# Kernel optimization log

Measured on AMD Instinct MI355X. Metric: run time of the kernel, lower is better.

The kernel has to match this reference:

```python
import jax, jax.numpy as jnp
import numpy as np

B, IN, HID, LAT, EH = 32768, 512, 2048, 128, 512
MID = max(HID // 2, LAT * 2)      # 1024
HALF = max(EH // 2, 4)            # 256
EPS = 1e-5
LN10 = float(np.log(10.0))


def setup_inputs() -> dict:
    key = jax.random.key(0)
    ks = jax.random.split(key, 24)
    r = lambda k, shp, s=0.02: (jax.random.normal(k, shp, dtype=jnp.float32) * s)
    d = {
        "x": jax.random.normal(ks[0], (B, IN), dtype=jnp.float32),
        "group_idx": jax.random.randint(ks[1], (B,), 0, 3),
        # encoder: Linear(IN,HID)+BN+ELU, Linear(HID,MID)+BN+ELU, Linear(MID,LAT)
        "e_w1": r(ks[2], (HID, IN)), "e_b1": jnp.zeros((HID,), jnp.float32),
        "e_g1": jnp.ones((HID,), jnp.float32), "e_be1": jnp.zeros((HID,), jnp.float32),
        "e_w2": r(ks[3], (MID, HID)), "e_b2": jnp.zeros((MID,), jnp.float32),
        "e_g2": jnp.ones((MID,), jnp.float32), "e_be2": jnp.zeros((MID,), jnp.float32),
        "e_w3": r(ks[4], (LAT, MID)), "e_b3": jnp.zeros((LAT,), jnp.float32),
        # shared: Linear(LAT+IN,HID)+BN+ELU, Linear(HID,MID)+BN+ELU
        "s_w1": r(ks[5], (HID, LAT + IN)), "s_b1": jnp.zeros((HID,), jnp.float32),
        "s_g1": jnp.ones((HID,), jnp.float32), "s_be1": jnp.zeros((HID,), jnp.float32),
        "s_w2": r(ks[6], (MID, HID)), "s_b2": jnp.zeros((MID,), jnp.float32),
        "s_g2": jnp.ones((MID,), jnp.float32), "s_be2": jnp.zeros((MID,), jnp.float32),
        # 3 expert heads, stacked on leading axis E=3
        "h_w1": r(ks[7], (3, EH, MID)), "h_b1": jnp.zeros((3, EH), jnp.float32),
        "h_w2": r(ks[8], (3, HALF, EH)), "h_b2": jnp.zeros((3, HALF), jnp.float32),
        "h_w3": r(ks[9], (3, HALF)), "h_b3": jnp.zeros((3,), jnp.float32),
    }
    return d


def _bn(h, g, b):
    # BatchNorm1d in training mode: batch mean, biased batch var
    m = jnp.mean(h, axis=0)
    v = jnp.var(h, axis=0)
    return (h - m) * (g / jnp.sqrt(v + EPS)) + b


def _elu(h):
    return jax.nn.elu(h)


def reference(x, group_idx,
              e_w1, e_b1, e_g1, e_be1, e_w2, e_b2, e_g2, e_be2, e_w3, e_b3,
              s_w1, s_b1, s_g1, s_be1, s_w2, s_b2, s_g2, s_be2,
              h_w1, h_b1, h_w2, h_b2, h_w3, h_b3):
    # encoder
    h = _elu(_bn(x @ e_w1.T + e_b1, e_g1, e_be1))
    h = _elu(_bn(h @ e_w2.T + e_b2, e_g2, e_be2))
    latent = h @ e_w3.T + e_b3                              # [B, LAT]
    # shared trunk
    z = jnp.concatenate([latent, x], axis=-1)               # [B, LAT+IN]
    h = _elu(_bn(z @ s_w1.T + s_b1, s_g1, s_be1))
    hidden = _elu(_bn(h @ s_w2.T + s_b2, s_g2, s_be2))      # [B, MID]
    # expert heads: compute all 3 (tiny vs trunk), then select per-row group
    t1 = _elu(jnp.einsum('bm,ehm->ebh', hidden, h_w1) + h_b1[:, None, :])   # [3,B,EH]
    t2 = _elu(jnp.einsum('ebh,efh->ebf', t1, h_w2) + h_b2[:, None, :])      # [3,B,HALF]
    pred_all = jnp.einsum('ebf,ef->eb', t2, h_w3) + h_b3[:, None]           # [3,B]
    pred_raw = jnp.take_along_axis(pred_all, group_idx[None, :], axis=0)[0] # [B]
    pred_log = -jax.nn.softplus(pred_raw)
    pred_prob = jnp.exp(pred_log * jnp.float32(LN10))       # 10 ** pred_log
    return pred_log, pred_prob
```

## Files before the change

kernel.cpp:

```cpp
#include <hip/hip_runtime.h>
#include <math.h>

#define B_    32768
#define LN10_ 2.302585092994046f
#define MT_H  264
#define NBLK  128

typedef __attribute__((ext_vector_type(8))) short short8;
typedef __attribute__((ext_vector_type(4))) float f32x4;

typedef const __attribute__((address_space(1))) void gvoid_t;
typedef __attribute__((address_space(3))) void svoid_t;

__device__ __forceinline__ void gl16(const void* g, void* l) {
  __builtin_amdgcn_global_load_lds((gvoid_t*)g, (svoid_t*)l, 16, 0, 0);
}

__device__ __forceinline__ float bf2f(unsigned int u) {
  union { unsigned int i; float f; } v; v.i = u << 16; return v.f;
}
__device__ __forceinline__ unsigned short f2bf(float f) {
  union { float f; unsigned int i; } v; v.f = f;
  unsigned int x = v.i;
  unsigned int r = x + 0x7FFFu + ((x >> 16) & 1u);
  return (unsigned short)(r >> 16);
}

#define SLB 16384

__global__ __launch_bounds__(512)
void gemm256(const unsigned short* __restrict__ A0, int lda,
             const unsigned short* __restrict__ W0, int ldw,
             unsigned short* __restrict__ C0, int ldc, int K,
             float* __restrict__ st, int Ntot) {
  __shared__ __align__(16) unsigned short lds[4 * SLB];
  const int t = threadIdx.x;
  const int nx = gridDim.x, ny = gridDim.y;
  const int f = blockIdx.y * nx + blockIdx.x;
  const int xcd = f & 7, g = f >> 3;
  const int gdiv = g / nx;
  const int mt = xcd * (ny >> 3) + gdiv;
  const int nt = g - gdiv * nx;
  const int mBase = mt * 256, nBase = nt * 256;
  const unsigned short* Ap = A0 + (size_t)mBase * lda;
  const unsigned short* Wp = W0 + (size_t)nBase * ldw;
  const int w = t >> 6, l = t & 63;
  const int wr = w >> 2, wc = w & 3;
  const int lm = l & 15, lg = l >> 4;

  const int srow = ((t >> 6) << 4) + (t & 15);
  const int skch = (t >> 4) & 3;
  const unsigned short* gA0 = Ap + (size_t)srow * lda + skch * 8;
  const unsigned short* gA1 = Ap + (size_t)(srow + 128) * lda + skch * 8;
  const unsigned short* gB0 = Wp + (size_t)srow * ldw + skch * 8;
  const unsigned short* gB1 = Wp + (size_t)(srow + 128) * ldw + skch * 8;

#define STAGE(ss)                                                         \
  {                                                                       \
    const int bo_ = ((ss) & 3) * SLB;                                     \
    const size_t ko_ = (size_t)(ss) * 32;                                 \
    gl16(gA0 + ko_, &lds[bo_ + t * 8]);                                   \
    gl16(gA1 + ko_, &lds[bo_ + 4096 + t * 8]);                            \
    gl16(gB0 + ko_, &lds[bo_ + 8192 + t * 8]);                            \
    gl16(gB1 + ko_, &lds[bo_ + 12288 + t * 8]);                           \
  }

  f32x4 acc[8][4];
#pragma unroll
  for (int i = 0; i < 8; ++i)
#pragma unroll
    for (int j = 0; j < 4; ++j) {
      f32x4 z4 = {0.f, 0.f, 0.f, 0.f};
      acc[i][j] = z4;
    }

  const int NS = K >> 5;
  STAGE(0); STAGE(1); STAGE(2);

#define GBODY(ss, dostage)                                                \
  {                                                                       \
    __builtin_amdgcn_s_barrier();                                         \
    __builtin_amdgcn_sched_barrier(0);                                    \
    const int bo = ((ss) & 3) * SLB;                                      \
    short8 af[8], bq[4];                                                  \
    _Pragma("unroll") for (int i = 0; i < 8; ++i)                         \
        af[i] = *(const short8*)&lds[bo + wr * 4096 + i * 512 + l * 8];   \
    _Pragma("unroll") for (int j = 0; j < 4; ++j)                         \
        bq[j] = *(const short8*)&lds[bo + 8192 + wc * 2048 + j * 512 + l * 8]; \
    if (dostage) STAGE((ss) + 3);                                         \
    __builtin_amdgcn_s_setprio(1);                                        \
    _Pragma("unroll") for (int i = 0; i < 8; ++i)                         \
      _Pragma("unroll") for (int j = 0; j < 4; ++j)                       \
        acc[i][j] = __builtin_amdgcn_mfma_f32_16x16x32_bf16(af[i], bq[j], acc[i][j], 0, 0, 0); \
    __builtin_amdgcn_s_setprio(0);                                        \
  }

  for (int s = 0; s + 2 < NS; ++s) {
    asm volatile("s_waitcnt vmcnt(8)" ::: "memory");
    GBODY(s, s + 3 < NS);
  }
  asm volatile("s_waitcnt vmcnt(4)" ::: "memory");
  GBODY(NS - 2, false);
  asm volatile("s_waitcnt vmcnt(0)" ::: "memory");
  GBODY(NS - 1, false);

#pragma unroll
  for (int j = 0; j < 4; ++j) {
    int n = nBase + wc * 64 + j * 16 + lm;
    float s1 = 0.f, q1 = 0.f;
#pragma unroll
    for (int i = 0; i < 8; ++i) {
      int m0 = mBase + wr * 128 + i * 16 + lg * 4;
#pragma unroll
      for (int r = 0; r < 4; ++r) {
        float v = acc[i][j][r];
        s1 += v; q1 += v * v;
        C0[(size_t)(m0 + r) * ldc + n] = f2bf(v);
      }
    }
    s1 += __shfl_xor(s1, 16, 64); s1 += __shfl_xor(s1, 32, 64);
    q1 += __shfl_xor(q1, 16, 64); q1 += __shfl_xor(q1, 32, 64);
    if (lg == 0) { atomicAdd(&st[n], s1); atomicAdd(&st[Ntot + n], q1); }
  }
}
#undef STAGE
#undef GBODY

__global__ __launch_bounds__(256)
void gemm_bt(const unsigned short* __restrict__ A0, int lda,
             const unsigned short* __restrict__ W0, int ldw,
             unsigned short* __restrict__ C0, int ldc,
             int K, const float* __restrict__ bias0, int elu,
             float* __restrict__ st, int Ntot,
             long eA, long eW, long eC, int eBias,
             const int* __restrict__ texp) {
  __shared__ __align__(16) unsigned short lA[128 * 64];
  __shared__ __align__(16) unsigned short lB[128 * 64];
  const int t = threadIdx.x;
  const int nx = gridDim.x, ny = gridDim.y;
  const int f = blockIdx.y * nx + blockIdx.x;
  const int xcd = f & 7, g = f >> 3;
  const int gdiv = g / nx;
  const int mt = xcd * (ny >> 3) + gdiv;
  const int nt = g - gdiv * nx;
  const int mBase = mt * 128;
  const int nBase = nt * 128;
  int e = texp ? texp[mt] : (int)blockIdx.z;
  if (e < 0) return;
  const unsigned short* A = A0 + (size_t)e * eA;
  const unsigned short* W = W0 + (size_t)e * eW;
  unsigned short* C = C0 + (size_t)e * eC;
  const float* bias = bias0 ? (bias0 + (size_t)e * eBias) : nullptr;
  const unsigned short* Ap = A + (size_t)mBase * lda;
  const unsigned short* Wp = W + (size_t)nBase * ldw;
  const int w = t >> 6, l = t & 63;
  const int wr = (w >> 1) * 64, wc = (w & 1) * 64;
  const int lm = l & 15, lg = l >> 4;

  f32x4 acc[4][4];
#pragma unroll
  for (int i = 0; i < 4; ++i)
#pragma unroll
    for (int j = 0; j < 4; ++j) {
      f32x4 z4 = {0.f, 0.f, 0.f, 0.f};
      acc[i][j] = z4;
    }

  for (int k0 = 0; k0 < K; k0 += 64) {
    __syncthreads();
#pragma unroll
    for (int it = 0; it < 4; ++it) {
      int chunk = it * 256 + t;
      int row = chunk >> 3, sc = chunk & 7;
      int gc = (sc ^ (row & 7)) << 3;
      gl16(Ap + (size_t)row * lda + k0 + gc, &lA[chunk * 8]);
      gl16(Wp + (size_t)row * ldw + k0 + gc, &lB[chunk * 8]);
    }
    __syncthreads();
#pragma unroll
    for (int kk = 0; kk < 64; kk += 32) {
      short8 af[4], bfr[4];
#pragma unroll
      for (int i = 0; i < 4; ++i) {
        int ar = wr + i * 16 + lm;
        int ac = (kk >> 3) + lg;
        af[i] = *(const short8*)&lA[ar * 64 + ((ac ^ (ar & 7)) << 3)];
      }
#pragma unroll
      for (int j = 0; j < 4; ++j) {
        int br = wc + j * 16 + lm;
        int bc = (kk >> 3) + lg;
        bfr[j] = *(const short8*)&lB[br * 64 + ((bc ^ (br & 7)) << 3)];
      }
#pragma unroll
      for (int i = 0; i < 4; ++i)
#pragma unroll
        for (int j = 0; j < 4; ++j)
          acc[i][j] = __builtin_amdgcn_mfma_f32_16x16x32_bf16(af[i], bfr[j], acc[i][j], 0, 0, 0);
    }
  }

#pragma unroll
  for (int j = 0; j < 4; ++j) {
    int n = nBase + wc + j * 16 + lm;
    float bj = bias ? bias[n] : 0.f;
    float s = 0.f, q = 0.f;
#pragma unroll
    for (int i = 0; i < 4; ++i) {
      int m0 = mBase + wr + i * 16 + lg * 4;
#pragma unroll
      for (int r = 0; r < 4; ++r) {
        float v = acc[i][j][r] + bj;
        if (elu) v = v > 0.f ? v : expm1f(v);
        s += v; q += v * v;
        C[(size_t)(m0 + r) * ldc + n] = f2bf(v);
      }
    }
    if (st) {
      s += __shfl_xor(s, 16, 64); s += __shfl_xor(s, 32, 64);
      q += __shfl_xor(q, 16, 64); q += __shfl_xor(q, 32, 64);
      if (lg == 0) { atomicAdd(&st[n], s); atomicAdd(&st[Ntot + n], q); }
    }
  }
}

__global__ void bn_apply(unsigned short* __restrict__ Y, const float* __restrict__ st,
                         const float* __restrict__ gam, const float* __restrict__ bet,
                         int N, float invB) {
  size_t i = (size_t)blockIdx.x * blockDim.x + threadIdx.x;
  size_t base = i * 8;
  int col = (int)(base & (size_t)(N - 1));
  float a8[8], b8[8];
#pragma unroll
  for (int k = 0; k < 8; ++k) {
    int c = col + k;
    float m = st[c] * invB;
    float var = st[N + c] * invB - m * m;
    float av = gam[c] * rsqrtf(var + 1e-5f);
    a8[k] = av;
    b8[k] = bet[c] - m * av;
  }
  uint4 u = *(uint4*)&Y[base];
  unsigned int uu[4] = {u.x, u.y, u.z, u.w};
  unsigned int oo[4];
#pragma unroll
  for (int k = 0; k < 4; ++k) {
    float vlo = bf2f(uu[k] & 0xFFFFu);
    float vhi = bf2f(uu[k] >> 16);
    float flo = a8[2 * k] * vlo + b8[2 * k];
    float fhi = a8[2 * k + 1] * vhi + b8[2 * k + 1];
    flo = flo > 0.f ? flo : expm1f(flo);
    fhi = fhi > 0.f ? fhi : expm1f(fhi);
    oo[k] = (unsigned int)f2bf(flo) | ((unsigned int)f2bf(fhi) << 16);
  }
  uint4 o = {oo[0], oo[1], oo[2], oo[3]};
  *(uint4*)&Y[base] = o;
}

__global__ void cast_all(const float* __restrict__ e1, const float* __restrict__ e2,
                         const float* __restrict__ e3, const float* __restrict__ s1,
                         const float* __restrict__ s2, const float* __restrict__ h1,
                         const float* __restrict__ h2, unsigned short* __restrict__ dst) {
  int i4 = blockIdx.x * 256 + threadIdx.x;
  const float* src;
  int rel;
  if (i4 < 786432) {
    if (i4 < 262144) { src = e1; rel = i4; }
    else             { src = e2; rel = i4 - 262144; }
  } else if (i4 < 1146880) {
    if (i4 < 819200) { src = e3; rel = i4 - 786432; }
    else             { src = s1; rel = i4 - 819200; }
  } else if (i4 < 2064384) {
    if (i4 < 1671168) { src = s2; rel = i4 - 1146880; }
    else              { src = h1; rel = i4 - 1671168; }
  } else { src = h2; rel = i4 - 2064384; }
  float4 v = ((const float4*)src)[rel];
  ushort4 o = {f2bf(v.x), f2bf(v.y), f2bf(v.z), f2bf(v.w)};
  ((ushort4*)dst)[i4] = o;
}

__global__ void cast_x(const float* __restrict__ x, unsigned short* __restrict__ z) {
  int i = blockIdx.x * blockDim.x + threadIdx.x;
  int b = i >> 7;
  int c = (i & 127) << 2;
  float4 v = *(const float4*)&x[(size_t)b * 512 + c];
  ushort4 o = {f2bf(v.x), f2bf(v.y), f2bf(v.z), f2bf(v.w)};
  *(ushort4*)&z[(size_t)b * 640 + 128 + c] = o;
}

__global__ void hist_blocks(const int* __restrict__ gidx, int* __restrict__ bcnt) {
  int blk = blockIdx.x;
  int i = blk * 256 + threadIdx.x;
  int e = gidx[i];
  int l = threadIdx.x & 63, w = threadIdx.x >> 6;
  __shared__ int wc[4][3];
  unsigned long long m0 = __ballot(e == 0);
  unsigned long long m1 = __ballot(e == 1);
  unsigned long long m2 = __ballot(e == 2);
  if (l == 0) { wc[w][0] = __popcll(m0); wc[w][1] = __popcll(m1); wc[w][2] = __popcll(m2); }
  __syncthreads();
  if (threadIdx.x < 3)
    bcnt[blk * 3 + threadIdx.x] = wc[0][threadIdx.x] + wc[1][threadIdx.x] +
                                  wc[2][threadIdx.x] + wc[3][threadIdx.x];
}

__global__ void scan_plan(const int* __restrict__ bcnt, int* __restrict__ boff,
                          int* __restrict__ vend, int* __restrict__ texp) {
  __shared__ int sp[4];
  __shared__ int cnt[3];
  int t = threadIdx.x;
  if (t < 3) {
    int s = 0;
    for (int b = 0; b < NBLK; ++b) s += bcnt[b * 3 + t];
    cnt[t] = s;
  }
  __syncthreads();
  if (t == 0) {
    int p = 0;
    for (int e = 0; e < 3; ++e) {
      sp[e] = p; vend[e] = p + cnt[e];
      p += ((cnt[e] + 127) >> 7) << 7;
    }
    sp[3] = p;
  }
  __syncthreads();
  if (t < 3) {
    int run = sp[t];
    for (int b = 0; b < NBLK; ++b) { boff[b * 3 + t] = run; run += bcnt[b * 3 + t]; }
  }
  if (t < MT_H) {
    int r0 = t << 7, e = -1;
    for (int k = 0; k < 3; ++k)
      if (r0 >= sp[k] && r0 < sp[k + 1]) e = k;
    texp[t] = e;
  }
}

__global__ void scatter2(const int* __restrict__ gidx, const int* __restrict__ boff,
                         int* __restrict__ perm) {
  int blk = blockIdx.x;
  int i = blk * 256 + threadIdx.x;
  int e = gidx[i];
  int l = threadIdx.x & 63, w = threadIdx.x >> 6;
  __shared__ int wc[4][3];
  unsigned long long m0 = __ballot(e == 0);
  unsigned long long m1 = __ballot(e == 1);
  unsigned long long m2 = __ballot(e == 2);
  if (l == 0) { wc[w][0] = __popcll(m0); wc[w][1] = __popcll(m1); wc[w][2] = __popcll(m2); }
  __syncthreads();
  unsigned long long me = (e == 0) ? m0 : ((e == 1) ? m1 : m2);
  int rank = __popcll(me & ((1ull << l) - 1ull));
  int woff = 0;
  for (int ww = 0; ww < w; ++ww) woff += wc[ww][e];
  perm[boff[blk * 3 + e] + woff + rank] = i;
}

__global__ void gather_h(const unsigned short* __restrict__ hid, const int* __restrict__ perm,
                         const int* __restrict__ texp, const int* __restrict__ vend,
                         unsigned short* __restrict__ ht) {
  int idx = blockIdx.x * 256 + threadIdx.x;
  int p = idx >> 7, c8 = (idx & 127) << 3;
  int e = texp[p >> 7];
  uint4 v = {0u, 0u, 0u, 0u};
  if (e >= 0 && p < vend[e]) {
    int src = perm[p];
    v = *(const uint4*)&hid[(size_t)src * 1024 + c8];
  }
  *(uint4*)&ht[(size_t)p * 1024 + c8] = v;
}

__global__ void final_pred(const unsigned short* __restrict__ t2, const int* __restrict__ perm,
                           const int* __restrict__ texp, const int* __restrict__ vend,
                           const float* __restrict__ w3, const float* __restrict__ b3,
                           float* __restrict__ out) {
  int p = blockIdx.x * 4 + (threadIdx.x >> 6);
  int l = threadIdx.x & 63;
  int e = texp[p >> 7];
  if (e < 0 || p >= vend[e]) return;
  ushort4 u = *(const ushort4*)&t2[(size_t)p * 256 + l * 4];
  float4 wv = *(const float4*)&w3[e * 256 + l * 4];
  float sum = bf2f(u.x) * wv.x + bf2f(u.y) * wv.y + bf2f(u.z) * wv.z + bf2f(u.w) * wv.w;
#pragma unroll
  for (int off = 32; off; off >>= 1) sum += __shfl_down(sum, off, 64);
  if (l == 0) {
    int orig = perm[p];
    float xr = sum + b3[e];
    float sp = (xr > 0.f) ? (xr + log1pf(expf(-xr))) : log1pf(expf(xr));
    float pl = -sp;
    out[orig] = pl;
    out[B_ + orig] = expf(pl * LN10_);
  }
}

extern "C" void kernel_launch(void* const* d_in, const int* in_sizes, int n_in,
                              void* d_out, int out_size, void* d_ws, size_t ws_size,
                              hipStream_t stream) {
  const float* x    = (const float*)d_in[0];
  const int*   gidx = (const int*)d_in[1];
  const float* e_w1 = (const float*)d_in[2];
  const float* e_g1 = (const float*)d_in[4];
  const float* e_be1= (const float*)d_in[5];
  const float* e_w2 = (const float*)d_in[6];
  const float* e_g2 = (const float*)d_in[8];
  const float* e_be2= (const float*)d_in[9];
  const float* e_w3 = (const float*)d_in[10];
  const float* e_b3 = (const float*)d_in[11];
  const float* s_w1 = (const float*)d_in[12];
  const float* s_g1 = (const float*)d_in[14];
  const float* s_be1= (const float*)d_in[15];
  const float* s_w2 = (const float*)d_in[16];
  const float* s_g2 = (const float*)d_in[18];
  const float* s_be2= (const float*)d_in[19];
  const float* h_w1 = (const float*)d_in[20];
  const float* h_b1 = (const float*)d_in[21];
  const float* h_w2 = (const float*)d_in[22];
  const float* h_b2 = (const float*)d_in[23];
  const float* h_w3 = (const float*)d_in[24];
  const float* h_b3 = (const float*)d_in[25];
  float* out = (float*)d_out;

  char* ws = (char*)d_ws;
  size_t off = 0;
  auto alloc = [&](size_t bytes) -> char* {
    char* p = ws + off;
    off += (bytes + 255) & ~(size_t)255;
    return p;
  };
  unsigned short* wb_e1 = (unsigned short*)alloc((size_t)2048 * 512 * 2);
  unsigned short* wb_e2 = (unsigned short*)alloc((size_t)1024 * 2048 * 2);
  unsigned short* wb_e3 = (unsigned short*)alloc((size_t)128 * 1024 * 2);
  unsigned short* wb_s1 = (unsigned short*)alloc((size_t)2048 * 640 * 2);
  unsigned short* wb_s2 = (unsigned short*)alloc((size_t)1024 * 2048 * 2);
  unsigned short* wb_h1 = (unsigned short*)alloc((size_t)3 * 512 * 1024 * 2);
  unsigned short* wb_h2 = (unsigned short*)alloc((size_t)3 * 256 * 512 * 2);
  unsigned short* z     = (unsigned short*)alloc((size_t)B_ * 640 * 2);
  unsigned short* bufA  = (unsigned short*)alloc((size_t)B_ * 2048 * 2);
  unsigned short* bufB  = (unsigned short*)alloc((size_t)B_ * 1024 * 2);
  float* st = (float*)alloc(12288 * sizeof(float));
  float* st0 = st;
  float* st1 = st + 4096;
  float* st2 = st + 6144;
  float* st3 = st + 10240;
  int* bcnt = (int*)alloc(NBLK * 3 * sizeof(int));
  int* boff = (int*)alloc(NBLK * 3 * sizeof(int));
  int* vend = (int*)alloc(3 * sizeof(int));
  int* texp = (int*)alloc(MT_H * sizeof(int));
  int* perm = (int*)alloc((size_t)MT_H * 128 * sizeof(int));
  unsigned short* ht  = bufA;
  unsigned short* t1p = bufA + (size_t)MT_H * 128 * 1024;
  unsigned short* t2p = z;

  cast_all<<<8448, 256, 0, stream>>>(e_w1, e_w2, e_w3, s_w1, s_w2, h_w1, h_w2, wb_e1);
  cast_x<<<(B_ * 128) / 256, 256, 0, stream>>>(x, z);
  hipMemsetAsync(st, 0, 12288 * sizeof(float), stream);
  hist_blocks<<<NBLK, 256, 0, stream>>>(gidx, bcnt);
  scan_plan<<<1, 512, 0, stream>>>(bcnt, boff, vend, texp);
  scatter2<<<NBLK, 256, 0, stream>>>(gidx, boff, perm);

  gemm256<<<dim3(8, 128), 512, 0, stream>>>(z + 128, 640, wb_e1, 512, bufA, 2048, 512,
                                            st0, 2048);
  bn_apply<<<B_, 256, 0, stream>>>(bufA, st0, e_g1, e_be1, 2048, 1.0f / B_);
  gemm256<<<dim3(4, 128), 512, 0, stream>>>(bufA, 2048, wb_e2, 2048, bufB, 1024, 2048,
                                            st1, 1024);
  bn_apply<<<B_ / 2, 256, 0, stream>>>(bufB, st1, e_g2, e_be2, 1024, 1.0f / B_);
  gemm_bt<<<dim3(1, 256), 256, 0, stream>>>(bufB, 1024, wb_e3, 1024, z, 640, 1024,
                                            e_b3, 0, nullptr, 0, 0, 0, 0, 0, nullptr);
  gemm256<<<dim3(8, 128), 512, 0, stream>>>(z, 640, wb_s1, 640, bufA, 2048, 640,
                                            st2, 2048);
  bn_apply<<<B_, 256, 0, stream>>>(bufA, st2, s_g1, s_be1, 2048, 1.0f / B_);
  gemm256<<<dim3(4, 128), 512, 0, stream>>>(bufA, 2048, wb_s2, 2048, bufB, 1024, 2048,
                                            st3, 1024);
  bn_apply<<<B_ / 2, 256, 0, stream>>>(bufB, st3, s_g2, s_be2, 1024, 1.0f / B_);

  gather_h<<<(MT_H * 128 * 128) / 256, 256, 0, stream>>>(bufB, perm, texp, vend, ht);

  gemm_bt<<<dim3(4, MT_H), 256, 0, stream>>>(ht, 1024, wb_h1, 1024, t1p, 512, 1024,
                                             h_b1, 1, nullptr, 0,
                                             0, (long)512 * 1024, 0, 512, texp);
  gemm_bt<<<dim3(2, MT_H), 256, 0, stream>>>(t1p, 512, wb_h2, 512, t2p, 256, 512,
                                             h_b2, 1, nullptr, 0,
                                             0, (long)256 * 512, 0, 256, texp);

  final_pred<<<(MT_H * 128) / 4, 256, 0, stream>>>(t2p, perm, texp, vend, h_w3, h_b3, out);
}
```

Baseline: 1.102 ms.

## Restructure gemm256 to K=64 double-buffered tiles with XOR-swizzled LDS layout

Replaces the 4-stage K=32 pipeline, which staged data in an MFMA-fragment-ordered layout, with a 2-stage double buffer of K=64 tiles stored row-major with an XOR swizzle on 16-byte chunks. Loads for the next tile are split into A and B halves and interleaved between the two K=32 MFMA sub-steps. The change is meant to make global loads more contiguous (full 128-byte row segments) and to cut the number of barriers. In exchange the pipeline depth drops and each iteration waits on vmcnt(0), so load latency may be exposed. The XOR swizzle also has to keep LDS reads free of bank conflicts.

Result: faster. 1.025 ms (-7.0%).

```diff
diff --git a/kernel.cpp b/kernel.cpp
--- a/kernel.cpp
+++ b/kernel.cpp
@@ -26,14 +26,14 @@
   return (unsigned short)(r >> 16);
 }
 
-#define SLB 16384
+#define TLA 16384
 
 __global__ __launch_bounds__(512)
 void gemm256(const unsigned short* __restrict__ A0, int lda,
              const unsigned short* __restrict__ W0, int ldw,
              unsigned short* __restrict__ C0, int ldc, int K,
              float* __restrict__ st, int Ntot) {
-  __shared__ __align__(16) unsigned short lds[4 * SLB];
+  __shared__ __align__(16) unsigned short lds[4 * TLA];
   const int t = threadIdx.x;
   const int nx = gridDim.x, ny = gridDim.y;
   const int f = blockIdx.y * nx + blockIdx.x;
@@ -48,22 +48,32 @@
   const int wr = w >> 2, wc = w & 3;
   const int lm = l & 15, lg = l >> 4;
 
-  const int srow = ((t >> 6) << 4) + (t & 15);
-  const int skch = (t >> 4) & 3;
-  const unsigned short* gA0 = Ap + (size_t)srow * lda + skch * 8;
-  const unsigned short* gA1 = Ap + (size_t)(srow + 128) * lda + skch * 8;
-  const unsigned short* gB0 = Wp + (size_t)srow * ldw + skch * 8;
-  const unsigned short* gB1 = Wp + (size_t)(srow + 128) * ldw + skch * 8;
-
-#define STAGE(ss)                                                         \
+  const int rr = t >> 3;
+  const int xc = ((t & 7) ^ (rr & 7)) << 3;
+  const unsigned short* gA = Ap + (size_t)rr * lda + xc;
+  const unsigned short* gB = Wp + (size_t)rr * ldw + xc;
+
+#define STAGE_A(tt)                                                       \
   {                                                                       \
-    const int bo_ = ((ss) & 3) * SLB;                                     \
-    const size_t ko_ = (size_t)(ss) * 32;                                 \
-    gl16(gA0 + ko_, &lds[bo_ + t * 8]);                                   \
-    gl16(gA1 + ko_, &lds[bo_ + 4096 + t * 8]);                            \
-    gl16(gB0 + ko_, &lds[bo_ + 8192 + t * 8]);                            \
-    gl16(gB1 + ko_, &lds[bo_ + 12288 + t * 8]);                           \
-  }
+    const int d_ = ((tt) & 1) * 2 * TLA;                                  \
+    const size_t ko_ = (size_t)(tt) * 64;                                 \
+    gl16(gA + ko_,                    &lds[d_ + t * 8]);                  \
+    gl16(gA + (size_t)64 * lda + ko_, &lds[d_ + 4096 + t * 8]);           \
+    gl16(gA + (size_t)128 * lda + ko_, &lds[d_ + 8192 + t * 8]);          \
+    gl16(gA + (size_t)192 * lda + ko_, &lds[d_ + 12288 + t * 8]);         \
+  }
+#define STAGE_B(tt)                                                       \
+  {                                                                       \
+    const int d_ = ((tt) & 1) * 2 * TLA + TLA;                            \
+    const size_t ko_ = (size_t)(tt) * 64;                                 \
+    gl16(gB + ko_,                    &lds[d_ + t * 8]);                  \
+    gl16(gB + (size_t)64 * ldw + ko_, &lds[d_ + 4096 + t * 8]);           \
+    gl16(gB + (size_t)128 * ldw + ko_, &lds[d_ + 8192 + t * 8]);          \
+    gl16(gB + (size_t)192 * ldw + ko_, &lds[d_ + 12288 + t * 8]);         \
+  }
+
+  const int cs0 = ((lg) ^ (l & 7)) << 3;
+  const int cs1 = ((4 | lg) ^ (l & 7)) << 3;
 
   f32x4 acc[8][4];
 #pragma unroll
@@ -74,35 +84,58 @@
       acc[i][j] = z4;
     }
 
-  const int NS = K >> 5;
-  STAGE(0); STAGE(1); STAGE(2);
-
-#define GBODY(ss, dostage)                                                \
-  {                                                                       \
-    __builtin_amdgcn_s_barrier();                                         \
-    __builtin_amdgcn_sched_barrier(0);                                    \
-    const int bo = ((ss) & 3) * SLB;                                      \
-    short8 af[8], bq[4];                                                  \
-    _Pragma("unroll") for (int i = 0; i < 8; ++i)                         \
-        af[i] = *(const short8*)&lds[bo + wr * 4096 + i * 512 + l * 8];   \
-    _Pragma("unroll") for (int j = 0; j < 4; ++j)                         \
-        bq[j] = *(const short8*)&lds[bo + 8192 + wc * 2048 + j * 512 + l * 8]; \
-    if (dostage) STAGE((ss) + 3);                                         \
-    __builtin_amdgcn_s_setprio(1);                                        \
-    _Pragma("unroll") for (int i = 0; i < 8; ++i)                         \
-      _Pragma("unroll") for (int j = 0; j < 4; ++j)                       \
-        acc[i][j] = __builtin_amdgcn_mfma_f32_16x16x32_bf16(af[i], bq[j], acc[i][j], 0, 0, 0); \
-    __builtin_amdgcn_s_setprio(0);                                        \
-  }
-
-  for (int s = 0; s + 2 < NS; ++s) {
-    asm volatile("s_waitcnt vmcnt(8)" ::: "memory");
-    GBODY(s, s + 3 < NS);
-  }
-  asm volatile("s_waitcnt vmcnt(4)" ::: "memory");
-  GBODY(NS - 2, false);
-  asm volatile("s_waitcnt vmcnt(0)" ::: "memory");
-  GBODY(NS - 1, false);
+  const int NT = K >> 6;
+  STAGE_A(0); STAGE_B(0);
+
+  for (int tt = 0; tt < NT; ++tt) {
+    asm volatile("s_waitcnt vmcnt(0)" ::: "memory");
+    __builtin_amdgcn_s_barrier();
+    __builtin_amdgcn_sched_barrier(0);
+    const int d = (tt & 1) * 2 * TLA;
+    const bool more = (tt + 1 < NT);
+    if (more) STAGE_A(tt + 1);
+    {
+      short8 af[8], bq[4];
+#pragma unroll
+      for (int i = 0; i < 8; ++i) {
+        int arow = wr * 128 + i * 16 + lm;
+        af[i] = *(const short8*)&lds[d + arow * 64 + cs0];
+      }
+#pragma unroll
+      for (int j = 0; j < 4; ++j) {
+        int brow = wc * 64 + j * 16 + lm;
+        bq[j] = *(const short8*)&lds[d + TLA + brow * 64 + cs0];
+      }
+      __builtin_amdgcn_s_setprio(1);
+#pragma unroll
+      for (int i = 0; i < 8; ++i)
+#pragma unroll
+        for (int j = 0; j < 4; ++j)
+          acc[i][j] = __builtin_amdgcn_mfma_f32_16x16x32_bf16(af[i], bq[j], acc[i][j], 0, 0, 0);
+      __builtin_amdgcn_s_setprio(0);
+    }
+    if (more) STAGE_B(tt + 1);
+    {
+      short8 af[8], bq[4];
+#pragma unroll
+      for (int i = 0; i < 8; ++i) {
+        int arow = wr * 128 + i * 16 + lm;
+        af[i] = *(const short8*)&lds[d + arow * 64 + cs1];
+      }
+#pragma unroll
+      for (int j = 0; j < 4; ++j) {
+        int brow = wc * 64 + j * 16 + lm;
+        bq[j] = *(const short8*)&lds[d + TLA + brow * 64 + cs1];
+      }
+      __builtin_amdgcn_s_setprio(1);
+#pragma unroll
+      for (int i = 0; i < 8; ++i)
+#pragma unroll
+        for (int j = 0; j < 4; ++j)
+          acc[i][j] = __builtin_amdgcn_mfma_f32_16x16x32_bf16(af[i], bq[j], acc[i][j], 0, 0, 0);
+      __builtin_amdgcn_s_setprio(0);
+    }
+  }
 
 #pragma unroll
   for (int j = 0; j < 4; ++j) {
@@ -123,8 +156,8 @@
     if (lg == 0) { atomicAdd(&st[n], s1); atomicAdd(&st[Ntot + n], q1); }
   }
 }
-#undef STAGE
-#undef GBODY
+#undef STAGE_A
+#undef STAGE_B
 
 __global__ __launch_bounds__(256)
 void gemm_bt(const unsigned short* __restrict__ A0, int lda,
```
